# Optimization experiments

Measured on AMD Instinct MI355X. Metric: run time of the kernel, lower is better.

The kernel has to match this reference:

```python
import jax, jax.numpy as jnp
import numpy as np

D = 1024          # input_dim == output_dim == key_size
SLOTS = 128       # memory_slots
HID = 128         # write_heads hidden width
EPS = 1e-5        # LayerNorm eps (torch default)
WRITE_STRENGTH = 0.1


def _layernorm(x, g, b):
    mu = jnp.mean(x, axis=-1, keepdims=True)
    var = jnp.var(x, axis=-1, keepdims=True)
    return (x - mu) * jax.lax.rsqrt(var + EPS) * g + b


def setup_inputs() -> dict:
    key = jax.random.key(0)
    ks = jax.random.split(key, 12)
    B, S = 8, 4096
    xavier = float(np.sqrt(6.0 / (SLOTS + D)))
    return {
        "x": jax.random.normal(ks[0], (B, S, D), dtype=jnp.float32),
        "keys": jax.random.uniform(ks[1], (SLOTS, D), jnp.float32, -xavier, xavier),
        # original inits values to zeros but they become nonzero after writes; use small randn for a meaningful read
        "values": jax.random.normal(ks[2], (SLOTS, D), dtype=jnp.float32) * 0.02,
        "temperature": jnp.array([0.1], dtype=jnp.float32),
        "W1": jax.random.normal(ks[3], (D, HID), dtype=jnp.float32) * 0.02,
        "b1": jnp.zeros((HID,), jnp.float32),
        "W2": jax.random.normal(ks[4], (HID, SLOTS), dtype=jnp.float32) * 0.02,
        "b2": jnp.zeros((SLOTS,), jnp.float32),
        "Wf": jax.random.normal(ks[5], (2 * D, D), dtype=jnp.float32) * 0.02,
        "bf": jnp.zeros((D,), jnp.float32),
        "ln1_g": jnp.ones((D,), jnp.float32),
        "ln1_b": jnp.zeros((D,), jnp.float32),
        "Wo": jax.random.normal(ks[6], (D, D), dtype=jnp.float32) * 0.02,
        "bo": jnp.zeros((D,), jnp.float32),
        "ln2_g": jnp.ones((D,), jnp.float32),
        "ln2_b": jnp.zeros((D,), jnp.float32),
    }


def reference(x, keys, values, temperature, W1, b1, W2, b2, Wf, bf,
              ln1_g, ln1_b, Wo, bo, ln2_g, ln2_b):
    identity = x
    # proj_in is Identity since input_dim == output_dim
    q = x.reshape(-1, D)                                     # [N, D]
    # --- memory read: content-addressed softmax attention over SLOTS ---
    temp = jnp.clip(temperature, 1e-6, None)                 # clamp(min=1e-6)
    attn = jax.nn.softmax(q @ keys.T / temp, axis=-1)        # [N, SLOTS]
    mem_read = (attn @ values).reshape(x.shape)              # [B, S, D]
    # --- memory write (detached state update in the original) ---
    ww = jax.nn.sigmoid(jax.nn.gelu(q @ W1 + b1, approximate=False) @ W2 + b2)  # [N, SLOTS]
    new_values = values + WRITE_STRENGTH * (ww.T @ q)        # [SLOTS, D]
    # --- fusion + LN + Linear (+Dropout in eval mode = identity) ---
    fused = jnp.concatenate([x, mem_read], axis=-1) @ Wf + bf
    out = _layernorm(fused, ln1_g, ln1_b) @ Wo + bo
    # residual + post norm
    out = _layernorm(out + identity, ln2_g, ln2_b)
    return out, new_values
```

## Files before the change

### kernel.cpp

```cpp
#include <hip/hip_runtime.h>
#include <stdint.h>
#include <math.h>

typedef float f32x4 __attribute__((ext_vector_type(4)));
typedef __bf16 bf16x8_t __attribute__((ext_vector_type(8)));
typedef unsigned short us8 __attribute__((ext_vector_type(8)));
typedef unsigned short us4 __attribute__((ext_vector_type(4)));
typedef unsigned int u32;

__device__ __forceinline__ unsigned short f2bf(float f) {
  union { float f; uint32_t u; } v; v.f = f;
  uint32_t u = v.u;
  uint32_t r = (u + 0x7fffu + ((u >> 16) & 1u)) >> 16;
  return (unsigned short)r;
}
__device__ __forceinline__ float bf2f(unsigned short h) {
  union { uint32_t u; float f; } v; v.u = ((uint32_t)h) << 16;
  return v.f;
}
__device__ __forceinline__ f32x4 mfma16(us8 a, us8 b, f32x4 c) {
  return __builtin_amdgcn_mfma_f32_16x16x32_bf16(
      __builtin_bit_cast(bf16x8_t, a), __builtin_bit_cast(bf16x8_t, b), c, 0, 0, 0);
}
__device__ __forceinline__ void gl16(const void* g, void* l) {
  __builtin_amdgcn_global_load_lds(
      (const __attribute__((address_space(1))) u32*)g,
      (__attribute__((address_space(3))) u32*)l, 16, 0, 0);
}


__global__ __launch_bounds__(256) void k_tr(
    const float* __restrict__ src, unsigned short* __restrict__ dst,
    int R, int C, int dstride)
{
  __shared__ unsigned short X[64][68];
  int tile = blockIdx.x;
  int tpr = C >> 6;
  int tr = tile / tpr, tc = tile % tpr;
  int t = threadIdx.x;
  int r = t >> 2, c0 = (t & 3) * 16;
  const float* sp = src + (size_t)(tr * 64 + r) * C + tc * 64 + c0;
  #pragma unroll
  for (int q = 0; q < 4; ++q) {
    f32x4 v = *(const f32x4*)(sp + q * 4);
    us4 o;
    #pragma unroll
    for (int e = 0; e < 4; ++e) o[e] = f2bf(v[e]);
    *(us4*)&X[r][c0 + q * 4] = o;
  }
  __syncthreads();
  int o = t >> 2, k0 = (t & 3) * 16;
  us8 w0, w1;
  #pragma unroll
  for (int e = 0; e < 8; ++e) { w0[e] = X[k0 + e][o]; w1[e] = X[k0 + 8 + e][o]; }
  unsigned short* dp = dst + (size_t)(tc * 64 + o) * dstride + tr * 64 + k0;
  *(us8*)dp = w0;
  *(us8*)(dp + 8) = w1;
}

__global__ __launch_bounds__(256) void k_prep_small(
    const float* __restrict__ keys, const float* __restrict__ values,
    unsigned short* __restrict__ klw1, unsigned short* __restrict__ valB)
{
  int i = blockIdx.x * 256 + threadIdx.x;
  if (i < 131072) { klw1[i] = f2bf(keys[i]); return; }
  i -= 131072;
  valB[i] = f2bf(values[i]);
}

__global__ __launch_bounds__(256) void k_castx(
    const float* __restrict__ x, unsigned short* __restrict__ xb)
{
  size_t idx = ((size_t)blockIdx.x * 256 + threadIdx.x) * 8;
  f32x4 v0 = *(const f32x4*)(x + idx);
  f32x4 v1 = *(const f32x4*)(x + idx + 4);
  us8 o;
  #pragma unroll
  for (int e = 0; e < 4; ++e) { o[e] = f2bf(v0[e]); o[e + 4] = f2bf(v1[e]); }
  *(us8*)(xb + idx) = o;
}

template<int KTOT, int MT, int NTILES, int EPI, int KSPLIT = KTOT>
__global__ __launch_bounds__(512, 2) void k_gemm(
    const unsigned short* __restrict__ A, int astride,
    const unsigned short* __restrict__ A2, int astride2,
    const unsigned short* __restrict__ B,
    const float* __restrict__ bias,
    unsigned short* __restrict__ outB, float* __restrict__ outF,
    int ostride, int ocol,
    const unsigned short* __restrict__ residB)
{
  constexpr int NT = KTOT / 64;
  constexpr int AHW = MT * 64;
  constexpr int BUFHW = AHW + 16384;
  constexpr int AJ = MT / 64;
  constexpr int IFR = MT / 32;
  __shared__ __align__(16) unsigned short L[2 * BUFHW];

  int t = threadIdx.x;
  int bid = blockIdx.x;
  int logical;
  if (gridDim.x & 7) {
    logical = bid;
  } else {
    int cpx = gridDim.x >> 3;
    logical = (bid & 7) * cpx + (bid >> 3);
  }
  int m0 = (logical / NTILES) * MT, n0 = (logical % NTILES) * 256;

  int srow = t >> 3;
  int gslot = (t & 7) ^ (srow & 7);

  int w = t >> 6, l = t & 63, g = l >> 4, lc = l & 15;
  int wm = w >> 2, wn = w & 3;

  f32x4 acc[IFR][4] = {};

  auto stage = [&](int p, int kt) {
    int koff = kt * 64;
    const unsigned short* Ap = A; int astr = astride;
    if constexpr (KSPLIT < KTOT) {
      if (koff >= KSPLIT) { Ap = A2; astr = astride2; koff -= KSPLIT; }
    }
    int offa = koff + gslot * 8;
    int offb = kt * 64 + gslot * 8;
    #pragma unroll
    for (int j = 0; j < AJ; ++j)
      gl16(Ap + (size_t)(m0 + j * 64 + srow) * astr + offa,
           L + p * BUFHW + (j * 64 + srow) * 64 + (t & 7) * 8);
    #pragma unroll
    for (int j = 0; j < 4; ++j)
      gl16(B + (size_t)(n0 + j * 64 + srow) * KTOT + offb,
           L + p * BUFHW + AHW + (j * 64 + srow) * 64 + (t & 7) * 8);
  };

  stage(0, 0);
  if (NT > 1) stage(1, 1);

  for (int kt = 0; kt < NT; ++kt) {
    int p = kt & 1;
    if (kt + 1 < NT) {
      if constexpr (AJ + 4 == 6) asm volatile("s_waitcnt vmcnt(6)" ::: "memory");
      else                       asm volatile("s_waitcnt vmcnt(8)" ::: "memory");
    } else {
      asm volatile("s_waitcnt vmcnt(0)" ::: "memory");
    }
    __builtin_amdgcn_s_barrier();

    const unsigned short* Ab = L + p * BUFHW;
    const unsigned short* Bb = L + p * BUFHW + AHW;
    #pragma unroll
    for (int ks = 0; ks < 2; ++ks) {
      us8 av[IFR], bv[4];
      #pragma unroll
      for (int i = 0; i < IFR; ++i) {
        int row = wm * (MT / 2) + i * 16 + lc;
        av[i] = *(const us8*)(Ab + row * 64 + (((ks * 4 + g) ^ (lc & 7)) * 8));
      }
      #pragma unroll
      for (int j = 0; j < 4; ++j) {
        int row = wn * 64 + j * 16 + lc;
        bv[j] = *(const us8*)(Bb + row * 64 + (((ks * 4 + g) ^ (lc & 7)) * 8));
      }
      __builtin_amdgcn_s_setprio(1);
      #pragma unroll
      for (int i = 0; i < IFR; ++i)
        #pragma unroll
        for (int j = 0; j < 4; ++j)
          acc[i][j] = mfma16(av[i], bv[j], acc[i][j]);
      __builtin_amdgcn_s_setprio(0);
    }
    __builtin_amdgcn_s_barrier();
    if (kt + 2 < NT) stage(p, kt + 2);
  }

  float bv4[4];
  if constexpr (EPI == 0 || EPI == 5) {
    #pragma unroll
    for (int jn = 0; jn < 4; ++jn) bv4[jn] = bias[n0 + wn * 64 + jn * 16 + lc];
  }
  #pragma unroll
  for (int i = 0; i < IFR; ++i) {
    #pragma unroll
    for (int jj = 0; jj < 4; ++jj) {
      int row = m0 + wm * (MT / 2) + i * 16 + g * 4 + jj;
      #pragma unroll
      for (int jn = 0; jn < 4; ++jn) {
        int col = n0 + wn * 64 + jn * 16 + lc;
        float v = acc[i][jn][jj];
        if constexpr (EPI == 0 || EPI == 5) v += bv4[jn];
        if constexpr (EPI == 5) v += bf2f(residB[(size_t)row * 1024 + col]);
        if constexpr (EPI == 4) {
          outB[(size_t)col * 1152 + 1024 + row] = f2bf(v);
        } else {
          size_t oa = (size_t)row * ostride + ocol + col;
          if constexpr (EPI == 0 || EPI == 5) outB[oa] = f2bf(v);
          else                                outF[oa] = v;
        }
      }
    }
  }
}

__global__ __launch_bounds__(256) void k_smx(
    const float* __restrict__ lg, const float* __restrict__ b1,
    const float* __restrict__ b2, const float* __restrict__ temp,
    const unsigned short* __restrict__ w2t,
    unsigned short* __restrict__ attn, unsigned short* __restrict__ ww)
{
  __shared__ float lgs[16][260];
  __shared__ unsigned short hl[16][136];
  int t = threadIdx.x;
  int row0 = blockIdx.x * 16;

  {
    int r = t >> 4, c0 = (t & 15) * 16;
    const float* p = lg + (size_t)(row0 + r) * 256 + c0;
    #pragma unroll
    for (int q = 0; q < 4; ++q)
      *(f32x4*)&lgs[r][c0 + q * 4] = *(const f32x4*)(p + q * 4);
  }
  __syncthreads();

  {
    int r = t >> 4, sub = t & 15;
    float invt = 1.f / fmaxf(temp[0], 1e-6f);
    float vals[8]; float m = -3.4e38f;
    #pragma unroll
    for (int i = 0; i < 8; ++i) { vals[i] = lgs[r][sub * 8 + i]; m = fmaxf(m, vals[i]); }
    m = fmaxf(m, __shfl_xor(m, 1)); m = fmaxf(m, __shfl_xor(m, 2));
    m = fmaxf(m, __shfl_xor(m, 4)); m = fmaxf(m, __shfl_xor(m, 8));
    float ev[8]; float s = 0.f;
    #pragma unroll
    for (int i = 0; i < 8; ++i) { ev[i] = __expf((vals[i] - m) * invt); s += ev[i]; }
    s += __shfl_xor(s, 1); s += __shfl_xor(s, 2);
    s += __shfl_xor(s, 4); s += __shfl_xor(s, 8);
    float rinv = 1.f / s;
    us8 av;
    #pragma unroll
    for (int i = 0; i < 8; ++i) av[i] = f2bf(ev[i] * rinv);
    *(us8*)(attn + (size_t)(row0 + r) * 128 + sub * 8) = av;
    #pragma unroll
    for (int i = 0; i < 8; ++i) {
      float v = lgs[r][128 + sub * 8 + i] + b1[sub * 8 + i];
      v = 0.5f * v * (1.f + erff(v * 0.70710678118654752f));
      hl[r][sub * 8 + i] = f2bf(v);
    }
  }
  __syncthreads();

  int w = t >> 6, l = t & 63, g = l >> 4, lc = l & 15;
  int q2 = w * 2;
  f32x4 acc[2] = {};
  #pragma unroll
  for (int ks = 0; ks < 4; ++ks) {
    us8 a = *(const us8*)&hl[lc][ks * 32 + g * 8];
    #pragma unroll
    for (int i = 0; i < 2; ++i) {
      us8 b = *(const us8*)(w2t + (size_t)((q2 + i) * 16 + lc) * 128 + ks * 32 + g * 8);
      acc[i] = mfma16(a, b, acc[i]);
    }
  }
  #pragma unroll
  for (int i = 0; i < 2; ++i) {
    int col = (q2 + i) * 16 + lc;
    float bb = b2[col];
    #pragma unroll
    for (int j = 0; j < 4; ++j) {
      int r = row0 + g * 4 + j;
      float v = acc[i][j] + bb;
      v = 1.f / (1.f + __expf(-v));
      ww[(size_t)r * 128 + col] = f2bf(v);
    }
  }
}

__global__ __launch_bounds__(256) void k_wv(
    const unsigned short* __restrict__ xb, const unsigned short* __restrict__ ww,
    float* __restrict__ partials)
{
  __shared__ unsigned short wwT[128][40];
  __shared__ unsigned short xT[128][40];
  int t = threadIdx.x;
  int chunk = blockIdx.x >> 3;
  int dt0 = (blockIdx.x & 7) * 128;
  int w = t >> 6, l = t & 63, g = l >> 4, lc = l & 15;
  f32x4 acc[2][8] = {};
  int nn = t >> 3, e0 = (t & 7) * 16;

  for (int ks = 0; ks < 16; ++ks) {
    int n0 = chunk * 512 + ks * 32;
    __syncthreads();
    {
      us8 v0 = *(const us8*)(ww + (size_t)(n0 + nn) * 128 + e0);
      us8 v1 = *(const us8*)(ww + (size_t)(n0 + nn) * 128 + e0 + 8);
      #pragma unroll
      for (int i = 0; i < 8; ++i) { wwT[e0 + i][nn] = v0[i]; wwT[e0 + 8 + i][nn] = v1[i]; }
      const unsigned short* xp = xb + (size_t)(n0 + nn) * 1024 + dt0 + e0;
      us8 x0 = *(const us8*)xp;
      us8 x1 = *(const us8*)(xp + 8);
      #pragma unroll
      for (int i = 0; i < 8; ++i) { xT[e0 + i][nn] = x0[i]; xT[e0 + 8 + i][nn] = x1[i]; }
    }
    __syncthreads();
    us8 bfr[8];
    #pragma unroll
    for (int i = 0; i < 8; ++i) bfr[i] = *(const us8*)&xT[i * 16 + lc][g * 8];
    #pragma unroll
    for (int st = 0; st < 2; ++st) {
      us8 a = *(const us8*)&wwT[(w * 2 + st) * 16 + lc][g * 8];
      #pragma unroll
      for (int i = 0; i < 8; ++i) acc[st][i] = mfma16(a, bfr[i], acc[st][i]);
    }
  }
  float* p = partials + (size_t)chunk * 131072;
  #pragma unroll
  for (int st = 0; st < 2; ++st)
    #pragma unroll
    for (int i = 0; i < 8; ++i)
      #pragma unroll
      for (int j = 0; j < 4; ++j) {
        int s = (w * 2 + st) * 16 + g * 4 + j;
        p[s * 1024 + dt0 + i * 16 + lc] = acc[st][i][j];
      }
}

__global__ __launch_bounds__(256) void k_red(
    const float* __restrict__ values, const float* __restrict__ partials,
    float* __restrict__ outv)
{
  int i = blockIdx.x * 256 + threadIdx.x;
  float s = 0.f;
  #pragma unroll
  for (int c = 0; c < 64; ++c) s += partials[(size_t)c * 131072 + i];
  outv[i] = values[i] + 0.1f * s;
}

__global__ __launch_bounds__(256) void k_ln1(
    unsigned short* __restrict__ fb,
    const float* __restrict__ g, const float* __restrict__ b)
{
  int w = threadIdx.x >> 6, l = threadIdx.x & 63;
  int row = blockIdx.x * 4 + w;
  unsigned short* p = fb + (size_t)row * 1024 + l * 16;
  us8 v0 = *(const us8*)p;
  us8 v1 = *(const us8*)(p + 8);
  float vf[16];
  float s = 0.f, sq = 0.f;
  #pragma unroll
  for (int e = 0; e < 8; ++e) { vf[e] = bf2f(v0[e]); vf[e + 8] = bf2f(v1[e]); }
  #pragma unroll
  for (int e = 0; e < 16; ++e) { s += vf[e]; sq += vf[e] * vf[e]; }
  #pragma unroll
  for (int msk = 1; msk < 64; msk <<= 1) {
    s += __shfl_xor(s, msk); sq += __shfl_xor(sq, msk);
  }
  float mu = s * (1.f / 1024.f);
  float rs = rsqrtf(sq * (1.f / 1024.f) - mu * mu + 1e-5f);
  float gv[16], bv[16];
  #pragma unroll
  for (int q = 0; q < 4; ++q) {
    *(f32x4*)&gv[q * 4] = *(const f32x4*)(g + l * 16 + q * 4);
    *(f32x4*)&bv[q * 4] = *(const f32x4*)(b + l * 16 + q * 4);
  }
  us8 o0, o1;
  #pragma unroll
  for (int e = 0; e < 8; ++e) {
    o0[e] = f2bf((vf[e] - mu) * rs * gv[e] + bv[e]);
    o1[e] = f2bf((vf[e + 8] - mu) * rs * gv[e + 8] + bv[e + 8]);
  }
  *(us8*)p = o0;
  *(us8*)(p + 8) = o1;
}

__global__ __launch_bounds__(256) void k_ln2(
    const unsigned short* __restrict__ tp,
    const float* __restrict__ g, const float* __restrict__ b,
    float* __restrict__ out)
{
  int w = threadIdx.x >> 6, l = threadIdx.x & 63;
  int row = blockIdx.x * 4 + w;
  size_t base = (size_t)row * 1024 + l * 16;
  us8 t0 = *(const us8*)(tp + base);
  us8 t1 = *(const us8*)(tp + base + 8);
  float vf[16];
  #pragma unroll
  for (int e = 0; e < 8; ++e) { vf[e] = bf2f(t0[e]); vf[e + 8] = bf2f(t1[e]); }
  float s = 0.f, sq = 0.f;
  #pragma unroll
  for (int e = 0; e < 16; ++e) { s += vf[e]; sq += vf[e] * vf[e]; }
  #pragma unroll
  for (int msk = 1; msk < 64; msk <<= 1) {
    s += __shfl_xor(s, msk); sq += __shfl_xor(sq, msk);
  }
  float mu = s * (1.f / 1024.f);
  float rs = rsqrtf(sq * (1.f / 1024.f) - mu * mu + 1e-5f);
  #pragma unroll
  for (int q = 0; q < 4; ++q) {
    f32x4 gv = *(const f32x4*)(g + l * 16 + q * 4);
    f32x4 bv = *(const f32x4*)(b + l * 16 + q * 4);
    f32x4 o;
    #pragma unroll
    for (int e = 0; e < 4; ++e)
      o[e] = (vf[q * 4 + e] - mu) * rs * gv[e] + bv[e];
    *(f32x4*)(out + base + q * 4) = o;
  }
}

extern "C" void kernel_launch(void* const* d_in, const int* in_sizes, int n_in,
                              void* d_out, int out_size, void* d_ws, size_t ws_size,
                              hipStream_t stream) {
  const float* x      = (const float*)d_in[0];
  const float* keys   = (const float*)d_in[1];
  const float* values = (const float*)d_in[2];
  const float* temp   = (const float*)d_in[3];
  const float* W1     = (const float*)d_in[4];
  const float* b1     = (const float*)d_in[5];
  const float* W2     = (const float*)d_in[6];
  const float* b2     = (const float*)d_in[7];
  const float* Wf     = (const float*)d_in[8];
  const float* bfp    = (const float*)d_in[9];
  const float* ln1g   = (const float*)d_in[10];
  const float* ln1b   = (const float*)d_in[11];
  const float* Wo     = (const float*)d_in[12];
  const float* bo     = (const float*)d_in[13];
  const float* ln2g   = (const float*)d_in[14];
  const float* ln2b   = (const float*)d_in[15];

  char* ws = (char*)d_ws;
  unsigned short* wfb   = (unsigned short*)(ws + 0);
  unsigned short* shW   = (unsigned short*)(ws + 2359296);
  unsigned short* klw1  = (unsigned short*)(ws + 4456448);
  unsigned short* w2t   = (unsigned short*)(ws + 4980736);
  unsigned short* valB  = (unsigned short*)(ws + 5013504);
  unsigned short* attn  = (unsigned short*)(ws + 5275648);
  unsigned short* ww    = (unsigned short*)(ws + 13664256);
  float* lg             = (float*)(ws + 22052864);
  float* partials       = (float*)(ws + 22052864);
  unsigned short* tprime = (unsigned short*)(ws + 22052864);

  unsigned short* fb    = (unsigned short*)d_out;
  unsigned short* xb    = (unsigned short*)((char*)d_out + 67108864);
  float* out            = (float*)d_out;
  float* newvals        = (float*)((char*)d_out + 134217728);

  k_tr<<<256, 256, 0, stream>>>(Wf, wfb, 1024, 1024, 1152);
  k_tr<<<256, 256, 0, stream>>>(Wf + 1048576, shW, 1024, 1024, 1024);
  k_tr<<<32, 256, 0, stream>>>(W1, klw1 + 131072, 1024, 128, 1024);
  k_tr<<<4, 256, 0, stream>>>(W2, w2t, 128, 128, 128);
  k_prep_small<<<1024, 256, 0, stream>>>(keys, values, klw1, valB);
  k_castx<<<16384, 256, 0, stream>>>(x, xb);

  k_gemm<1024, 128, 4, 4><<<4, 512, 0, stream>>>(
      valB, 1024, nullptr, 0, shW, nullptr, wfb, nullptr, 0, 0, nullptr);
  k_tr<<<256, 256, 0, stream>>>(Wo, shW, 1024, 1024, 1024);

  k_gemm<1024, 128, 1, 2><<<256, 512, 0, stream>>>(
      xb, 1024, nullptr, 0, klw1, nullptr, nullptr, lg, 256, 0, nullptr);
  k_smx<<<2048, 256, 0, stream>>>(lg, b1, b2, temp, w2t, attn, ww);

  k_wv<<<512, 256, 0, stream>>>(xb, ww, partials);
  k_red<<<512, 256, 0, stream>>>(values, partials, newvals);

  k_gemm<1152, 256, 4, 0, 1024><<<512, 512, 0, stream>>>(
      xb, 1024, attn, 128, wfb, bfp, fb, nullptr, 1024, 0, nullptr);
  k_ln1<<<8192, 256, 0, stream>>>(fb, ln1g, ln1b);

  k_gemm<1024, 256, 4, 5><<<512, 512, 0, stream>>>(
      fb, 1024, nullptr, 0, shW, bo, tprime, nullptr, 1024, 0, xb);
  k_ln2<<<8192, 256, 0, stream>>>(tprime, ln2g, ln2b, out);
}
```

Before: 405.8 us.

## Fold LayerNorm1 into Wo GEMM via row stats and precomputed gamma/beta vectors

Removes the standalone LN1 pass over the fused activations. The fusion GEMM epilogue now emits per-row partial sums and sums of squares, which a small kernel reduces to mean and rstd. The output GEMM applies LN algebraically: gamma is scaled into Wo during transposition, and a GEMV precomputes gamma·Wo and beta·Wo+bo for the mean correction. This saves a full read/write of a 32K×1024 bf16 tensor. The trade-off is extra epilogue work and a mean-subtraction done after the GEMM, which may cost precision. The k_wv chunking is also changed to halve the number of blocks and partials.

```diff
diff --git a/kernel.cpp b/kernel.cpp
--- a/kernel.cpp
+++ b/kernel.cpp
@@ -31,7 +31,7 @@
 
 __global__ __launch_bounds__(256) void k_tr(
     const float* __restrict__ src, unsigned short* __restrict__ dst,
-    int R, int C, int dstride)
+    int R, int C, int dstride, const float* __restrict__ sc)
 {
   __shared__ unsigned short X[64][68];
   int tile = blockIdx.x;
@@ -39,13 +39,14 @@
   int tr = tile / tpr, tc = tile % tpr;
   int t = threadIdx.x;
   int r = t >> 2, c0 = (t & 3) * 16;
+  float s = sc ? sc[tr * 64 + r] : 1.f;
   const float* sp = src + (size_t)(tr * 64 + r) * C + tc * 64 + c0;
   #pragma unroll
   for (int q = 0; q < 4; ++q) {
     f32x4 v = *(const f32x4*)(sp + q * 4);
     us4 o;
     #pragma unroll
-    for (int e = 0; e < 4; ++e) o[e] = f2bf(v[e]);
+    for (int e = 0; e < 4; ++e) o[e] = f2bf(v[e] * s);
     *(us4*)&X[r][c0 + q * 4] = o;
   }
   __syncthreads();
@@ -66,6 +67,23 @@
   if (i < 131072) { klw1[i] = f2bf(keys[i]); return; }
   i -= 131072;
   valB[i] = f2bf(values[i]);
+}
+
+__global__ __launch_bounds__(256) void k_gemv(
+    const float* __restrict__ Wo, const float* __restrict__ g,
+    const float* __restrict__ b, const float* __restrict__ bo,
+    float* __restrict__ vg, float* __restrict__ cb)
+{
+  int o = blockIdx.x * 256 + threadIdx.x;
+  float sg = 0.f, sb = 0.f;
+  #pragma unroll 8
+  for (int k = 0; k < 1024; ++k) {
+    float w = Wo[(size_t)k * 1024 + o];
+    sg += g[k] * w;
+    sb += b[k] * w;
+  }
+  vg[o] = sg;
+  cb[o] = sb + bo[o];
 }
 
 __global__ __launch_bounds__(256) void k_castx(
@@ -88,7 +106,9 @@
     const float* __restrict__ bias,
     unsigned short* __restrict__ outB, float* __restrict__ outF,
     int ostride, int ocol,
-    const unsigned short* __restrict__ residB)
+    const unsigned short* __restrict__ residB,
+    const float* __restrict__ stats, const float* __restrict__ vg,
+    const float* __restrict__ cb, float* __restrict__ part)
 {
   constexpr int NT = KTOT / 64;
   constexpr int AHW = MT * 64;
@@ -174,32 +194,70 @@
     if (kt + 2 < NT) stage(p, kt + 2);
   }
 
-  float bv4[4];
-  if constexpr (EPI == 0 || EPI == 5) {
+  float bv4[4], vg4[4], cb4[4];
+  if constexpr (EPI == 6) {
     #pragma unroll
     for (int jn = 0; jn < 4; ++jn) bv4[jn] = bias[n0 + wn * 64 + jn * 16 + lc];
+  }
+  if constexpr (EPI == 5) {
+    #pragma unroll
+    for (int jn = 0; jn < 4; ++jn) {
+      int col = n0 + wn * 64 + jn * 16 + lc;
+      vg4[jn] = vg[col];
+      cb4[jn] = cb[col];
+    }
   }
   #pragma unroll
   for (int i = 0; i < IFR; ++i) {
     #pragma unroll
     for (int jj = 0; jj < 4; ++jj) {
       int row = m0 + wm * (MT / 2) + i * 16 + g * 4 + jj;
+      float mu = 0.f, rs = 0.f;
+      if constexpr (EPI == 5) { mu = stats[row * 2]; rs = stats[row * 2 + 1]; }
+      float ssum = 0.f, ssq = 0.f;
       #pragma unroll
       for (int jn = 0; jn < 4; ++jn) {
         int col = n0 + wn * 64 + jn * 16 + lc;
         float v = acc[i][jn][jj];
-        if constexpr (EPI == 0 || EPI == 5) v += bv4[jn];
-        if constexpr (EPI == 5) v += bf2f(residB[(size_t)row * 1024 + col]);
+        if constexpr (EPI == 6) v += bv4[jn];
+        if constexpr (EPI == 5)
+          v = rs * v - mu * rs * vg4[jn] + cb4[jn] + bf2f(residB[(size_t)row * 1024 + col]);
         if constexpr (EPI == 4) {
           outB[(size_t)col * 1152 + 1024 + row] = f2bf(v);
         } else {
           size_t oa = (size_t)row * ostride + ocol + col;
-          if constexpr (EPI == 0 || EPI == 5) outB[oa] = f2bf(v);
+          if constexpr (EPI == 5 || EPI == 6) outB[oa] = f2bf(v);
           else                                outF[oa] = v;
         }
+        if constexpr (EPI == 6) { ssum += v; ssq += v * v; }
       }
-    }
-  }
+      if constexpr (EPI == 6) {
+        #pragma unroll
+        for (int msk = 1; msk < 16; msk <<= 1) {
+          ssum += __shfl_xor(ssum, msk); ssq += __shfl_xor(ssq, msk);
+        }
+        if (lc == 0) {
+          int strip = (n0 >> 6) + wn;
+          part[(size_t)row * 32 + strip * 2]     = ssum;
+          part[(size_t)row * 32 + strip * 2 + 1] = ssq;
+        }
+      }
+    }
+  }
+}
+
+__global__ __launch_bounds__(256) void k_statsred(
+    const float* __restrict__ part, float* __restrict__ stats)
+{
+  int row = blockIdx.x * 256 + threadIdx.x;
+  const float* p = part + (size_t)row * 32;
+  float S = 0.f, Q = 0.f;
+  #pragma unroll
+  for (int i = 0; i < 16; ++i) { S += p[2 * i]; Q += p[2 * i + 1]; }
+  float mu = S * (1.f / 1024.f);
+  float rs = rsqrtf(Q * (1.f / 1024.f) - mu * mu + 1e-5f);
+  stats[row * 2] = mu;
+  stats[row * 2 + 1] = rs;
 }
 
 __global__ __launch_bounds__(256) void k_smx(
@@ -288,8 +346,8 @@
   f32x4 acc[2][8] = {};
   int nn = t >> 3, e0 = (t & 7) * 16;
 
-  for (int ks = 0; ks < 16; ++ks) {
-    int n0 = chunk * 512 + ks * 32;
+  for (int ks = 0; ks < 32; ++ks) {
+    int n0 = chunk * 1024 + ks * 32;
     __syncthreads();
     {
       us8 v0 = *(const us8*)(ww + (size_t)(n0 + nn) * 128 + e0);
@@ -332,45 +390,8 @@
   int i = blockIdx.x * 256 + threadIdx.x;
   float s = 0.f;
   #pragma unroll
-  for (int c = 0; c < 64; ++c) s += partials[(size_t)c * 131072 + i];
+  for (int c = 0; c < 32; ++c) s += partials[(size_t)c * 131072 + i];
   outv[i] = values[i] + 0.1f * s;
-}
-
-__global__ __launch_bounds__(256) void k_ln1(
-    unsigned short* __restrict__ fb,
-    const float* __restrict__ g, const float* __restrict__ b)
-{
-  int w = threadIdx.x >> 6, l = threadIdx.x & 63;
-  int row = blockIdx.x * 4 + w;
-  unsigned short* p = fb + (size_t)row * 1024 + l * 16;
-  us8 v0 = *(const us8*)p;
-  us8 v1 = *(const us8*)(p + 8);
-  float vf[16];
-  float s = 0.f, sq = 0.f;
-  #pragma unroll
-  for (int e = 0; e < 8; ++e) { vf[e] = bf2f(v0[e]); vf[e + 8] = bf2f(v1[e]); }
-  #pragma unroll
-  for (int e = 0; e < 16; ++e) { s += vf[e]; sq += vf[e] * vf[e]; }
-  #pragma unroll
-  for (int msk = 1; msk < 64; msk <<= 1) {
-    s += __shfl_xor(s, msk); sq += __shfl_xor(sq, msk);
-  }
-  float mu = s * (1.f / 1024.f);
-  float rs = rsqrtf(sq * (1.f / 1024.f) - mu * mu + 1e-5f);
-  float gv[16], bv[16];
-  #pragma unroll
-  for (int q = 0; q < 4; ++q) {
-    *(f32x4*)&gv[q * 4] = *(const f32x4*)(g + l * 16 + q * 4);
-    *(f32x4*)&bv[q * 4] = *(const f32x4*)(b + l * 16 + q * 4);
-  }
-  us8 o0, o1;
-  #pragma unroll
-  for (int e = 0; e < 8; ++e) {
-    o0[e] = f2bf((vf[e] - mu) * rs * gv[e] + bv[e]);
-    o1[e] = f2bf((vf[e + 8] - mu) * rs * gv[e + 8] + bv[e + 8]);
-  }
-  *(us8*)p = o0;
-  *(us8*)(p + 8) = o1;
 }
 
 __global__ __launch_bounds__(256) void k_ln2(
@@ -433,40 +454,49 @@
   unsigned short* klw1  = (unsigned short*)(ws + 4456448);
   unsigned short* w2t   = (unsigned short*)(ws + 4980736);
   unsigned short* valB  = (unsigned short*)(ws + 5013504);
-  unsigned short* attn  = (unsigned short*)(ws + 5275648);
-  unsigned short* ww    = (unsigned short*)(ws + 13664256);
-  float* lg             = (float*)(ws + 22052864);
-  float* partials       = (float*)(ws + 22052864);
-  unsigned short* tprime = (unsigned short*)(ws + 22052864);
+  float* vg             = (float*)(ws + 5275648);
+  float* cb             = (float*)(ws + 5279744);
+  float* stats          = (float*)(ws + 5283840);
+  float* part           = (float*)(ws + 5545984);
+  unsigned short* attn  = (unsigned short*)(ws + 9740288);
+  unsigned short* ww    = (unsigned short*)(ws + 18128896);
+  float* lg             = (float*)(ws + 26517504);
+  float* partials       = (float*)(ws + 26517504);
+  unsigned short* tprime = (unsigned short*)(ws + 26517504);
 
   unsigned short* fb    = (unsigned short*)d_out;
   unsigned short* xb    = (unsigned short*)((char*)d_out + 67108864);
   float* out            = (float*)d_out;
   float* newvals        = (float*)((char*)d_out + 134217728);
 
-  k_tr<<<256, 256, 0, stream>>>(Wf, wfb, 1024, 1024, 1152);
-  k_tr<<<256, 256, 0, stream>>>(Wf + 1048576, shW, 1024, 1024, 1024);
-  k_tr<<<32, 256, 0, stream>>>(W1, klw1 + 131072, 1024, 128, 1024);
-  k_tr<<<4, 256, 0, stream>>>(W2, w2t, 128, 128, 128);
+  k_tr<<<256, 256, 0, stream>>>(Wf, wfb, 1024, 1024, 1152, nullptr);
+  k_tr<<<256, 256, 0, stream>>>(Wf + 1048576, shW, 1024, 1024, 1024, nullptr);
+  k_tr<<<32, 256, 0, stream>>>(W1, klw1 + 131072, 1024, 128, 1024, nullptr);
+  k_tr<<<4, 256, 0, stream>>>(W2, w2t, 128, 128, 128, nullptr);
   k_prep_small<<<1024, 256, 0, stream>>>(keys, values, klw1, valB);
   k_castx<<<16384, 256, 0, stream>>>(x, xb);
 
   k_gemm<1024, 128, 4, 4><<<4, 512, 0, stream>>>(
-      valB, 1024, nullptr, 0, shW, nullptr, wfb, nullptr, 0, 0, nullptr);
-  k_tr<<<256, 256, 0, stream>>>(Wo, shW, 1024, 1024, 1024);
+      valB, 1024, nullptr, 0, shW, nullptr, wfb, nullptr, 0, 0,
+      nullptr, nullptr, nullptr, nullptr, nullptr);
+  k_tr<<<256, 256, 0, stream>>>(Wo, shW, 1024, 1024, 1024, ln1g);
+  k_gemv<<<4, 256, 0, stream>>>(Wo, ln1g, ln1b, bo, vg, cb);
 
   k_gemm<1024, 128, 1, 2><<<256, 512, 0, stream>>>(
-      xb, 1024, nullptr, 0, klw1, nullptr, nullptr, lg, 256, 0, nullptr);
+      xb, 1024, nullptr, 0, klw1, nullptr, nullptr, lg, 256, 0,
+      nullptr, nullptr, nullptr, nullptr, nullptr);
   k_smx<<<2048, 256, 0, stream>>>(lg, b1, b2, temp, w2t, attn, ww);
 
-  k_wv<<<512, 256, 0, stream>>>(xb, ww, partials);
+  k_wv<<<256, 256, 0, stream>>>(xb, ww, partials);
   k_red<<<512, 256, 0, stream>>>(values, partials, newvals);
 
-  k_gemm<1152, 256, 4, 0, 1024><<<512, 512, 0, stream>>>(
-      xb, 1024, attn, 128, wfb, bfp, fb, nullptr, 1024, 0, nullptr);
-  k_ln1<<<8192, 256, 0, stream>>>(fb, ln1g, ln1b);
+  k_gemm<1152, 256, 4, 6, 1024><<<512, 512, 0, stream>>>(
+      xb, 1024, attn, 128, wfb, bfp, fb, nullptr, 1024, 0,
+      nullptr, nullptr, nullptr, nullptr, part);
+  k_statsred<<<128, 256, 0, stream>>>(part, stats);
 
   k_gemm<1024, 256, 4, 5><<<512, 512, 0, stream>>>(
-      fb, 1024, nullptr, 0, shW, bo, tprime, nullptr, 1024, 0, xb);
+      fb, 1024, nullptr, 0, shW, nullptr, tprime, nullptr, 1024, 0,
+      xb, stats, vg, cb, nullptr);
   k_ln2<<<8192, 256, 0, stream>>>(tprime, ln2g, ln2b, out);
 }
```

New measurement: 431.0 us. 6.2% more time.

## Fuse x bf16 cast into logits GEMM and merge weight prep kernels

Applied to the files above, without the earlier changes.

Drops the standalone x-to-bf16 cast kernel and adds a new logits GEMM (k_logx) that reads fp32 x directly, converts it in registers, writes xb as a side output and stages the tile in LDS for MFMA. The four weight transposes and the keys/values cast are merged into one launch, which removes several kernel launches. The write-value partial kernel now covers twice as many rows per block and launches half as many blocks, so the reduction sums half as many partials. The intent is to avoid one full pass that re-reads xb and to cut launch overhead. In exchange k_logx uses 64-row tiles, which may be less efficient than the previous GEMM tiling, and k_wv runs with lower parallelism.

```diff
diff --git a/kernel.cpp b/kernel.cpp
--- a/kernel.cpp
+++ b/kernel.cpp
@@ -29,15 +29,13 @@
 }
 
 
-__global__ __launch_bounds__(256) void k_tr(
+__device__ __forceinline__ void tr_tile(
     const float* __restrict__ src, unsigned short* __restrict__ dst,
-    int R, int C, int dstride)
+    int C, int dstride, int tile, int t)
 {
   __shared__ unsigned short X[64][68];
-  int tile = blockIdx.x;
   int tpr = C >> 6;
   int tr = tile / tpr, tc = tile % tpr;
-  int t = threadIdx.x;
   int r = t >> 2, c0 = (t & 3) * 16;
   const float* sp = src + (size_t)(tr * 64 + r) * C + tc * 64 + c0;
   #pragma unroll
@@ -53,31 +51,35 @@
   us8 w0, w1;
   #pragma unroll
   for (int e = 0; e < 8; ++e) { w0[e] = X[k0 + e][o]; w1[e] = X[k0 + 8 + e][o]; }
-  unsigned short* dp = dst + (size_t)(tc * 64 + o) * dstride + tr * 64 + k0;
+  unsigned short* dp = dst + (size_t)(tc * 64 + o) * dstride + (size_t)tr * 64 + k0;
   *(us8*)dp = w0;
   *(us8*)(dp + 8) = w1;
 }
 
-__global__ __launch_bounds__(256) void k_prep_small(
-    const float* __restrict__ keys, const float* __restrict__ values,
-    unsigned short* __restrict__ klw1, unsigned short* __restrict__ valB)
-{
-  int i = blockIdx.x * 256 + threadIdx.x;
+__global__ __launch_bounds__(256) void k_prep_all(
+    const float* __restrict__ Wf, const float* __restrict__ W1,
+    const float* __restrict__ W2, const float* __restrict__ keys,
+    const float* __restrict__ values,
+    unsigned short* __restrict__ wfb, unsigned short* __restrict__ shW,
+    unsigned short* __restrict__ klw1, unsigned short* __restrict__ w2t,
+    unsigned short* __restrict__ valB)
+{
+  int b = blockIdx.x, t = threadIdx.x;
+  if (b < 256)       { tr_tile(Wf,            wfb,            1024, 1152, b,       t); return; }
+  if (b < 512)       { tr_tile(Wf + 1048576,  shW,            1024, 1024, b - 256, t); return; }
+  if (b < 544)       { tr_tile(W1,            klw1 + 131072,  128,  1024, b - 512, t); return; }
+  if (b < 548)       { tr_tile(W2,            w2t,            128,  128,  b - 544, t); return; }
+  int i = (b - 548) * 256 + t;
   if (i < 131072) { klw1[i] = f2bf(keys[i]); return; }
   i -= 131072;
   valB[i] = f2bf(values[i]);
 }
 
-__global__ __launch_bounds__(256) void k_castx(
-    const float* __restrict__ x, unsigned short* __restrict__ xb)
-{
-  size_t idx = ((size_t)blockIdx.x * 256 + threadIdx.x) * 8;
-  f32x4 v0 = *(const f32x4*)(x + idx);
-  f32x4 v1 = *(const f32x4*)(x + idx + 4);
-  us8 o;
-  #pragma unroll
-  for (int e = 0; e < 4; ++e) { o[e] = f2bf(v0[e]); o[e + 4] = f2bf(v1[e]); }
-  *(us8*)(xb + idx) = o;
+__global__ __launch_bounds__(256) void k_tr(
+    const float* __restrict__ src, unsigned short* __restrict__ dst,
+    int C, int dstride)
+{
+  tr_tile(src, dst, C, dstride, blockIdx.x, threadIdx.x);
 }
 
 template<int KTOT, int MT, int NTILES, int EPI, int KSPLIT = KTOT>
@@ -202,6 +204,95 @@
   }
 }
 
+__global__ __launch_bounds__(512, 4) void k_logx(
+    const float* __restrict__ x, const unsigned short* __restrict__ klw1,
+    unsigned short* __restrict__ xb, float* __restrict__ lg)
+{
+  constexpr int NT = 16;
+  __shared__ __align__(16) unsigned short Al[2][4096];
+  __shared__ __align__(16) unsigned short Bl[2][16384];
+
+  int t = threadIdx.x;
+  int bid = blockIdx.x;
+  int cpx = gridDim.x >> 3;
+  int logical = (bid & 7) * cpx + (bid >> 3);
+  int m0 = logical * 64;
+
+  int ar = t >> 3, aq = t & 7;
+  int adst = ar * 64 + ((aq ^ (ar & 7)) * 8);
+  const float* axp = x + (size_t)(m0 + ar) * 1024 + aq * 8;
+  unsigned short* xbp = xb + (size_t)(m0 + ar) * 1024 + aq * 8;
+
+  int srow = t >> 3;
+  int gslot = (t & 7) ^ (srow & 7);
+
+  int w = t >> 6, l = t & 63, g = l >> 4, lc = l & 15;
+  int wm = w >> 2, wn = w & 3;
+
+  f32x4 acc[2][4] = {};
+  f32x4 a0, a1;
+
+  auto loadA = [&](int kt) {
+    a0 = *(const f32x4*)(axp + kt * 64);
+    a1 = *(const f32x4*)(axp + kt * 64 + 4);
+  };
+  auto stageB = [&](int p, int kt) {
+    #pragma unroll
+    for (int j = 0; j < 4; ++j)
+      gl16(klw1 + (size_t)(j * 64 + srow) * 1024 + kt * 64 + gslot * 8,
+           &Bl[p][(j * 64 + srow) * 64 + (t & 7) * 8]);
+  };
+
+  loadA(0);
+  stageB(0, 0);
+
+  for (int kt = 0; kt < NT; ++kt) {
+    int cur = kt & 1;
+    us8 av8;
+    #pragma unroll
+    for (int e = 0; e < 4; ++e) { av8[e] = f2bf(a0[e]); av8[e + 4] = f2bf(a1[e]); }
+    *(us8*)(xbp + kt * 64) = av8;
+    *(us8*)&Al[cur][adst] = av8;
+    __syncthreads();
+    if (kt + 1 < NT) {
+      loadA(kt + 1);
+      stageB(cur ^ 1, kt + 1);
+    }
+    #pragma unroll
+    for (int ks = 0; ks < 2; ++ks) {
+      us8 af[2], bf[4];
+      #pragma unroll
+      for (int i = 0; i < 2; ++i) {
+        int row = wm * 32 + i * 16 + lc;
+        af[i] = *(const us8*)&Al[cur][row * 64 + (((ks * 4 + g) ^ (lc & 7)) * 8)];
+      }
+      #pragma unroll
+      for (int j = 0; j < 4; ++j) {
+        int row = wn * 64 + j * 16 + lc;
+        bf[j] = *(const us8*)&Bl[cur][row * 64 + (((ks * 4 + g) ^ (lc & 7)) * 8)];
+      }
+      #pragma unroll
+      for (int i = 0; i < 2; ++i)
+        #pragma unroll
+        for (int j = 0; j < 4; ++j)
+          acc[i][j] = mfma16(af[i], bf[j], acc[i][j]);
+    }
+    __syncthreads();
+  }
+
+  #pragma unroll
+  for (int i = 0; i < 2; ++i)
+    #pragma unroll
+    for (int jj = 0; jj < 4; ++jj) {
+      int row = m0 + wm * 32 + i * 16 + g * 4 + jj;
+      #pragma unroll
+      for (int jn = 0; jn < 4; ++jn) {
+        int col = wn * 64 + jn * 16 + lc;
+        lg[(size_t)row * 256 + col] = acc[i][jn][jj];
+      }
+    }
+}
+
 __global__ __launch_bounds__(256) void k_smx(
     const float* __restrict__ lg, const float* __restrict__ b1,
     const float* __restrict__ b2, const float* __restrict__ temp,
@@ -288,8 +379,8 @@
   f32x4 acc[2][8] = {};
   int nn = t >> 3, e0 = (t & 7) * 16;
 
-  for (int ks = 0; ks < 16; ++ks) {
-    int n0 = chunk * 512 + ks * 32;
+  for (int ks = 0; ks < 32; ++ks) {
+    int n0 = chunk * 1024 + ks * 32;
     __syncthreads();
     {
       us8 v0 = *(const us8*)(ww + (size_t)(n0 + nn) * 128 + e0);
@@ -332,7 +423,7 @@
   int i = blockIdx.x * 256 + threadIdx.x;
   float s = 0.f;
   #pragma unroll
-  for (int c = 0; c < 64; ++c) s += partials[(size_t)c * 131072 + i];
+  for (int c = 0; c < 32; ++c) s += partials[(size_t)c * 131072 + i];
   outv[i] = values[i] + 0.1f * s;
 }
 
@@ -444,22 +535,17 @@
   float* out            = (float*)d_out;
   float* newvals        = (float*)((char*)d_out + 134217728);
 
-  k_tr<<<256, 256, 0, stream>>>(Wf, wfb, 1024, 1024, 1152);
-  k_tr<<<256, 256, 0, stream>>>(Wf + 1048576, shW, 1024, 1024, 1024);
-  k_tr<<<32, 256, 0, stream>>>(W1, klw1 + 131072, 1024, 128, 1024);
-  k_tr<<<4, 256, 0, stream>>>(W2, w2t, 128, 128, 128);
-  k_prep_small<<<1024, 256, 0, stream>>>(keys, values, klw1, valB);
-  k_castx<<<16384, 256, 0, stream>>>(x, xb);
+  k_prep_all<<<1572, 256, 0, stream>>>(Wf, W1, W2, keys, values,
+                                       wfb, shW, klw1, w2t, valB);
 
   k_gemm<1024, 128, 4, 4><<<4, 512, 0, stream>>>(
       valB, 1024, nullptr, 0, shW, nullptr, wfb, nullptr, 0, 0, nullptr);
-  k_tr<<<256, 256, 0, stream>>>(Wo, shW, 1024, 1024, 1024);
-
-  k_gemm<1024, 128, 1, 2><<<256, 512, 0, stream>>>(
-      xb, 1024, nullptr, 0, klw1, nullptr, nullptr, lg, 256, 0, nullptr);
+  k_tr<<<256, 256, 0, stream>>>(Wo, shW, 1024, 1024);
+
+  k_logx<<<512, 512, 0, stream>>>(x, klw1, xb, lg);
   k_smx<<<2048, 256, 0, stream>>>(lg, b1, b2, temp, w2t, attn, ww);
 
-  k_wv<<<512, 256, 0, stream>>>(xb, ww, partials);
+  k_wv<<<256, 256, 0, stream>>>(xb, ww, partials);
   k_red<<<512, 256, 0, stream>>>(values, partials, newvals);
 
   k_gemm<1152, 256, 4, 0, 1024><<<512, 512, 0, stream>>>(
```

Measured after the change: 388.1 us. 4.4% less time.
